# Kernel tuning notes

Hardware: AMD Instinct MI355X
Metric: run time of the kernel (lower is better)

## Reference

```python
import jax, jax.numpy as jnp
import numpy as np

N = 50000          # nodes
E = 3_200_000      # edges (radius-graph topology, avg degree ~64)
C = 10             # node channels
ED = 4             # edge_dim: [dist, dx, dy, food_flag]
H = 16             # message hidden dim
RADIUS = 0.05
ACC_SCALE = 0.005
MAX_VEL = 0.02
EDGES_TO_STAY_ALIVE = 3
CONSUMPTION_EDGES_REQUIRED = 3
NOISE_SCALE = 0.004


def setup_inputs() -> dict:
    key = jax.random.key(0)
    ks = jax.random.split(key, 10)
    pos = jax.random.uniform(ks[0], (N, 2), minval=-1.0, maxval=1.0)
    vel = jax.random.uniform(ks[1], (N, 2), minval=-MAX_VEL, maxval=MAX_VEL)
    # column 4: 1.0 = living cell, 0.0 = food node
    is_cell = (jax.random.uniform(ks[2], (N,)) > 0.2).astype(jnp.float32)
    hidden = jax.random.normal(ks[3], (N, C - 5)) * 0.1
    x = jnp.concatenate([pos, vel, is_cell[:, None], hidden], axis=1)  # [N,10]
    src = jax.random.randint(ks[4], (E,), 0, N)
    dst = jax.random.randint(ks[5], (E,), 0, N)
    noise = jax.random.uniform(ks[6], (N, 2))  # uniform [0,1), mapped to [-1,1) inside
    W_edge = jax.random.normal(ks[7], (ED, H)) * 0.3
    W_src = jax.random.normal(ks[8], (C, H)) * 0.3
    b1 = jnp.zeros((H,), jnp.float32)
    W_out = jax.random.normal(ks[9], (H, 4)) * 0.3
    b2 = jnp.zeros((4,), jnp.float32)
    return dict(x=x, src=src, dst=dst, noise=noise, W_edge=W_edge,
                W_src=W_src, b1=b1, W_out=W_out, b2=b2)


def reference(x, src, dst, noise, W_edge, W_src, b1, W_out, b2):
    pos = x[:, :2]
    vel = x[:, 2:4]
    cell = x[:, 4]
    c_mask = (cell == 1.0).astype(x.dtype)          # [N]

    # ---- edge attributes of the (dynamic) radius graph ----
    d = pos[src] - pos[dst]                          # [E,2] gather
    dist = jnp.sqrt(jnp.sum(d * d, axis=1) + 1e-12)  # [E]
    food_flag = cell[src]                            # 0 for food-source edges
    edge_attr = jnp.concatenate([dist[:, None], d, food_flag[:, None]], axis=1)  # [E,4]

    # ---- message passing: per-edge MLP + scatter-sum + node readout ----
    m = jax.nn.relu(edge_attr @ W_edge + x[src] @ W_src + b1)     # [E,H]
    agg = jax.ops.segment_sum(m, dst, num_segments=N)             # [N,H]
    h = jnp.tanh(agg @ W_out + b2) * c_mask[:, None]              # [N,4], masked as in update_graph

    # ---- velocity / position update ----
    acc = h[:, :2] * ACC_SCALE
    new_vel = jnp.clip(vel + acc, -MAX_VEL, MAX_VEL)
    new_pos = pos + new_vel                                       # wrap_around = False
    vel_noisy = new_vel + (noise * 2.0 - 1.0) * NOISE_SCALE * c_mask[:, None]
    new_x = jnp.concatenate(
        [new_pos, vel_noisy, cell[:, None], h[:, 2:], x[:, 7:]], axis=1)  # [N,10]

    # ---- costs / stats ----
    eps = 1e-6
    border_mask = (jnp.abs(new_pos) > 1.0).astype(x.dtype)        # [N,2]
    border_cost = jnp.sum(jnp.log(jnp.abs(new_pos) + eps) * border_mask)
    food_edge = (food_flag == 0.0)
    visible_food = food_edge.sum()
    mean_food_dist = jnp.sum(dist * food_edge.astype(x.dtype))

    # ---- node removal masks (jit-safe: return keep mask instead of slicing) ----
    deg = jax.ops.segment_sum(jnp.ones_like(dist), dst, num_segments=N)
    dead = (cell == 1.0) & (deg < EDGES_TO_STAY_ALIVE)
    consume_e = (dist < RADIUS) & (cell[src] == 1.0) & (cell[dst] == 0.0)
    cdeg = jax.ops.segment_sum(consume_e.astype(x.dtype), dst, num_segments=N)
    consumed = (cell == 0.0) & (cdeg >= CONSUMPTION_EDGES_REQUIRED)
    keep_mask = ~(dead | consumed)

    velocity_bonus = jnp.mean(jnp.abs(new_vel), axis=0)           # [2]
    dead_cost = dead.sum()
    food_reward = consumed.sum()
    return (new_x, keep_mask, velocity_bonus, border_cost, food_reward,
            dead_cost, visible_food, mean_food_dist)
```

## Files before the change

kernel.cpp:

```cpp
#include <hip/hip_runtime.h>
#include <hip/hip_fp16.h>
#include <math.h>

#define NN 50000
#define NE 3200000

#define NT    128
#define TSZ   392
#define CAP   26624
#define SCB   625
#define EPB   5120
#define EPT   20
#define NSL   6

static constexpr float ACC_SCALE   = 0.005f;
static constexpr float MAX_VEL     = 0.02f;
static constexpr float NOISE_SCALE = 0.004f;
static constexpr float RADIUS      = 0.05f;

#define OUT_KEEP   500000
#define OUT_SCAL   550000

#define WS_SREC  0
#define WS_GCUR  802816
#define WS_BK    804864
#define WS_PACC  4212736
#define WS_PDEG  5416960

__global__ __launch_bounds__(256) void k1_prep(
    const float* __restrict__ x,
    const float* __restrict__ W_edge,
    const float* __restrict__ W_src,
    const float* __restrict__ b1,
    float4* __restrict__ srec,
    int* __restrict__ gcur,
    float* __restrict__ out_scalars)
{
    int n = blockIdx.x * 256 + threadIdx.x;
    if (blockIdx.x == 0) {
        if (threadIdx.x < 7) out_scalars[threadIdx.x] = 0.0f;
        for (int i = threadIdx.x; i < NT * 16; i += 256)
            gcur[i] = (i & 15) ? 0 : (i >> 4) * CAP;
    }
    if (n >= NN) return;

    float xr[10];
#pragma unroll
    for (int c = 0; c < 10; ++c) xr[c] = x[n * 10 + c];
    float cell = xr[4];

    float v[16];
#pragma unroll
    for (int j = 0; j < 16; ++j) {
        float a = fmaf(cell, W_edge[48 + j], b1[j]);
#pragma unroll
        for (int c = 0; c < 10; ++c) a = fmaf(xr[c], W_src[c * 16 + j], a);
        v[j] = a;
    }

    float4 r1, r2;
    r1.x = __builtin_bit_cast(float, __floats2half2_rn(v[0],  v[1]));
    r1.y = __builtin_bit_cast(float, __floats2half2_rn(v[2],  v[3]));
    r1.z = __builtin_bit_cast(float, __floats2half2_rn(v[4],  v[5]));
    r1.w = __builtin_bit_cast(float, __floats2half2_rn(v[6],  v[7]));
    r2.x = __builtin_bit_cast(float, __floats2half2_rn(v[8],  v[9]));
    r2.y = __builtin_bit_cast(float, __floats2half2_rn(v[10], v[11]));
    r2.z = __builtin_bit_cast(float, __floats2half2_rn(v[12], v[13]));
    r2.w = __builtin_bit_cast(float, __floats2half2_rn(v[14], v[15]));

    srec[(size_t)n * 4 + 0] = make_float4(xr[0], xr[1], cell, 0.0f);
    srec[(size_t)n * 4 + 1] = r1;
    srec[(size_t)n * 4 + 2] = r2;
}

__global__ __launch_bounds__(256) void k_scatter(
    const int* __restrict__ src,
    const int* __restrict__ dst,
    int* __restrict__ gcur,
    unsigned* __restrict__ bucket)
{
    __shared__ unsigned stage[EPB];
    __shared__ int hist[NT], binstart[NT], lcur[NT], gbase[NT];
    __shared__ int scanbuf[128];

    int tid = threadIdx.x;
    for (int i = tid; i < NT; i += 256) { hist[i] = 0; lcur[i] = 0; }
    __syncthreads();

    int e0 = blockIdx.x * EPB;

    int d[EPT];
#pragma unroll
    for (int j = 0; j < EPT; ++j) d[j] = dst[e0 + j * 256 + tid];
#pragma unroll
    for (int j = 0; j < EPT; ++j) atomicAdd(&hist[d[j] / TSZ], 1);
    __syncthreads();

    if (tid < 128) scanbuf[tid] = hist[tid];
    __syncthreads();
    for (int off = 1; off < 128; off <<= 1) {
        int v = 0;
        if (tid < 128 && tid >= off) v = scanbuf[tid - off];
        __syncthreads();
        if (tid < 128) scanbuf[tid] += v;
        __syncthreads();
    }
    if (tid < 128) {
        int tt = (tid + blockIdx.x) & 127;
        int bs = scanbuf[tt] - hist[tt];
        binstart[tt] = bs;
        gbase[tt] = atomicAdd(&gcur[tt * 16], hist[tt]) - bs;
    }
    __syncthreads();

    int sreg[EPT];
#pragma unroll
    for (int j = 0; j < EPT; ++j) sreg[j] = src[e0 + j * 256 + tid];
#pragma unroll
    for (int j = 0; j < EPT; ++j) {
        int t  = d[j] / TSZ;
        int dl = d[j] - t * TSZ;
        int pos = binstart[t] + atomicAdd(&lcur[t], 1);
        stage[pos] = (unsigned)sreg[j] | ((unsigned)dl << 16)
                   | ((unsigned)t << 25);
    }
    __syncthreads();

#pragma unroll
    for (int j = 0; j < EPT; ++j) {
        int i = j * 256 + tid;
        unsigned e = stage[i];
        int b = e >> 25;
        int g = gbase[b] + i;
        if (g < (b + 1) * CAP) __builtin_nontemporal_store(e, &bucket[g]);
    }
}

__global__ __launch_bounds__(256, 2) void k_agg(
    const float* __restrict__ W_edge,
    const float* __restrict__ W_out,
    const float4* __restrict__ srec,
    const int* __restrict__ gcur,
    const unsigned* __restrict__ bucket,
    float4* __restrict__ pacc,
    int* __restrict__ pdeg,
    float* __restrict__ out_scalars)
{
    __shared__ float  sAcc[TSZ][5];
    __shared__ int    sDeg[TSZ];
    __shared__ float4 sNI[TSZ];
    __shared__ float  sRed[4][2];

    int t   = blockIdx.x / NSL;
    int sl  = blockIdx.x - t * NSL;
    int tid = threadIdx.x;

    for (int j = tid; j < TSZ; j += 256) {
        int g = t * TSZ + j;
        sNI[j] = (g < NN) ? srec[(size_t)g * 4]
                          : make_float4(9e9f, 9e9f, -1.f, 0.f);
        sAcc[j][0] = 0.f; sAcc[j][1] = 0.f; sAcc[j][2] = 0.f; sAcc[j][3] = 0.f;
        sDeg[j] = 0;
    }

    float w0[16], w1[16], w2[16], woa[16], wob[16], woc[16], wod[16];
#pragma unroll
    for (int k = 0; k < 16; ++k) {
        w0[k] = W_edge[k];
        w1[k] = W_edge[16 + k];
        w2[k] = W_edge[32 + k];
        woa[k] = W_out[k * 4 + 0];
        wob[k] = W_out[k * 4 + 1];
        woc[k] = W_out[k * 4 + 2];
        wod[k] = W_out[k * 4 + 3];
    }
    __syncthreads();

    int cnt = gcur[t * 16] - t * CAP;
    if (cnt > CAP) cnt = CAP;
    int per = (cnt + NSL - 1) / NSL;
    int i0 = sl * per;
    int i1 = min(i0 + per, cnt);

    const unsigned* bk = bucket + (size_t)t * CAP;
    float vis = 0.f, fd = 0.f;

    auto PROC = [&](unsigned e, float4 A, float4 B, float4 C) {
        int dl = (e >> 16) & 0x1FF;
        float4 ni = sNI[dl];
        float dx = A.x - ni.x;
        float dy = A.y - ni.y;
        float dist = sqrtf(fmaf(dx, dx, fmaf(dy, dy, 1e-12f)));

        bool food0 = (A.z == 0.0f);
        vis += food0 ? 1.f : 0.f;
        fd  += food0 ? dist : 0.f;

        bool consume = (dist < RADIUS) && (A.z == 1.0f) && (ni.z == 0.0f);
        atomicAdd(&sDeg[dl], consume ? 65537 : 1);

        float sv[16];
        float2 f;
        f = __half22float2(__builtin_bit_cast(__half2, B.x)); sv[0]=f.x;  sv[1]=f.y;
        f = __half22float2(__builtin_bit_cast(__half2, B.y)); sv[2]=f.x;  sv[3]=f.y;
        f = __half22float2(__builtin_bit_cast(__half2, B.z)); sv[4]=f.x;  sv[5]=f.y;
        f = __half22float2(__builtin_bit_cast(__half2, B.w)); sv[6]=f.x;  sv[7]=f.y;
        f = __half22float2(__builtin_bit_cast(__half2, C.x)); sv[8]=f.x;  sv[9]=f.y;
        f = __half22float2(__builtin_bit_cast(__half2, C.y)); sv[10]=f.x; sv[11]=f.y;
        f = __half22float2(__builtin_bit_cast(__half2, C.z)); sv[12]=f.x; sv[13]=f.y;
        f = __half22float2(__builtin_bit_cast(__half2, C.w)); sv[14]=f.x; sv[15]=f.y;

        float v0 = 0.f, v1 = 0.f, v2 = 0.f, v3 = 0.f;
#pragma unroll
        for (int k = 0; k < 16; ++k) {
            float m = fmaf(dist, w0[k], fmaf(dx, w1[k], fmaf(dy, w2[k], sv[k])));
            m = fmaxf(m, 0.0f);
            v0 = fmaf(m, woa[k], v0);
            v1 = fmaf(m, wob[k], v1);
            v2 = fmaf(m, woc[k], v2);
            v3 = fmaf(m, wod[k], v3);
        }
        atomicAdd(&sAcc[dl][0], v0);
        atomicAdd(&sAcc[dl][1], v1);
        atomicAdd(&sAcc[dl][2], v2);
        atomicAdd(&sAcc[dl][3], v3);
    };

#pragma unroll 1
    for (int base = i0 + tid; base < i1; base += 1024) {
        int iend = i1 - 1;
        int j1 = min(base + 256, iend);
        int j2 = min(base + 512, iend);
        int j3 = min(base + 768, iend);

        unsigned e0 = __builtin_nontemporal_load(&bk[base]);
        unsigned e1 = __builtin_nontemporal_load(&bk[j1]);
        unsigned e2 = __builtin_nontemporal_load(&bk[j2]);
        unsigned e3 = __builtin_nontemporal_load(&bk[j3]);

        const float4* p0 = srec + (size_t)(e0 & 0xFFFF) * 4;
        const float4* p1 = srec + (size_t)(e1 & 0xFFFF) * 4;
        const float4* p2 = srec + (size_t)(e2 & 0xFFFF) * 4;
        const float4* p3 = srec + (size_t)(e3 & 0xFFFF) * 4;
        float4 A0 = p0[0], B0 = p0[1], C0 = p0[2];
        float4 A1 = p1[0], B1 = p1[1], C1 = p1[2];
        float4 A2 = p2[0], B2 = p2[1], C2 = p2[2];
        float4 A3 = p3[0], B3 = p3[1], C3 = p3[2];

        PROC(e0, A0, B0, C0);
        if (base + 256 < i1) PROC(e1, A1, B1, C1);
        if (base + 512 < i1) PROC(e2, A2, B2, C2);
        if (base + 768 < i1) PROC(e3, A3, B3, C3);
    }
    __syncthreads();

    for (int j = tid; j < TSZ; j += 256) {
        int o = sl * (NT * TSZ) + t * TSZ + j;
        pacc[o] = make_float4(sAcc[j][0], sAcc[j][1], sAcc[j][2], sAcc[j][3]);
        pdeg[o] = sDeg[j];
    }

#pragma unroll
    for (int off = 32; off > 0; off >>= 1) {
        vis += __shfl_down(vis, off);
        fd  += __shfl_down(fd,  off);
    }
    int lane = tid & 63, wv = tid >> 6;
    if (lane == 0) { sRed[wv][0] = vis; sRed[wv][1] = fd; }
    __syncthreads();
    if (tid == 0) {
        float a = 0.f, b = 0.f;
#pragma unroll
        for (int wq = 0; wq < 4; ++wq) { a += sRed[wq][0]; b += sRed[wq][1]; }
        atomicAdd(&out_scalars[5], a);
        atomicAdd(&out_scalars[6], b);
    }
}

__global__ __launch_bounds__(256) void k_final(
    const float* __restrict__ x,
    const float* __restrict__ noise,
    const float* __restrict__ b2,
    const float4* __restrict__ pacc,
    const int* __restrict__ pdeg,
    float* __restrict__ out,
    float* __restrict__ out_scalars)
{
    __shared__ float sRed[4][5];
    int tid  = threadIdx.x;
    int n    = blockIdx.x * 128 + (tid >> 1);
    int half = tid & 1;

    float a0 = 0.f, a1 = 0.f, a2 = 0.f, a3 = 0.f;
    int dp = 0;
    if (n < NN) {
#pragma unroll
        for (int k = 0; k < NSL / 2; ++k) {
            int o = (2 * k + half) * (NT * TSZ) + n;
            float4 q = pacc[o];
            a0 += q.x; a1 += q.y; a2 += q.z; a3 += q.w;
            dp += pdeg[o];
        }
    }
    a0 += __shfl_xor(a0, 1);
    a1 += __shfl_xor(a1, 1);
    a2 += __shfl_xor(a2, 1);
    a3 += __shfl_xor(a3, 1);
    dp += __shfl_xor(dp, 1);

    float avx = 0.f, avy = 0.f, bc = 0.f, deadf = 0.f, consf = 0.f;
    if (n < NN && half == 0) {
        float cell = x[n * 10 + 4];
        float cm = (cell == 1.0f) ? 1.0f : 0.0f;
        float h0 = tanhf(a0 + b2[0]) * cm;
        float h1 = tanhf(a1 + b2[1]) * cm;
        float h2 = tanhf(a2 + b2[2]) * cm;
        float h3 = tanhf(a3 + b2[3]) * cm;

        float px = x[n * 10 + 0], py = x[n * 10 + 1];
        float vx = x[n * 10 + 2], vy = x[n * 10 + 3];

        float nvx = fminf(fmaxf(fmaf(h0, ACC_SCALE, vx), -MAX_VEL), MAX_VEL);
        float nvy = fminf(fmaxf(fmaf(h1, ACC_SCALE, vy), -MAX_VEL), MAX_VEL);
        float npx = px + nvx;
        float npy = py + nvy;

        float vnx = nvx + (noise[n * 2 + 0] * 2.0f - 1.0f) * NOISE_SCALE * cm;
        float vny = nvy + (noise[n * 2 + 1] * 2.0f - 1.0f) * NOISE_SCALE * cm;

        float* row = out + (size_t)n * 10;
        row[0] = npx;  row[1] = npy;
        row[2] = vnx;  row[3] = vny;
        row[4] = cell; row[5] = h2;  row[6] = h3;
        row[7] = x[n * 10 + 7];
        row[8] = x[n * 10 + 8];
        row[9] = x[n * 10 + 9];

        float apx = fabsf(npx), apy = fabsf(npy);
        if (apx > 1.0f) bc += logf(apx + 1e-6f);
        if (apy > 1.0f) bc += logf(apy + 1e-6f);

        int deg  = dp & 0xFFFF;
        int cdeg = dp >> 16;
        bool dead = (cell == 1.0f) && (deg < 3);
        bool cons = (cell == 0.0f) && (cdeg >= 3);
        out[OUT_KEEP + n] = (dead || cons) ? 0.0f : 1.0f;
        deadf = dead ? 1.0f : 0.0f;
        consf = cons ? 1.0f : 0.0f;
        avx = fabsf(nvx) * (1.0f / NN);
        avy = fabsf(nvy) * (1.0f / NN);
    }

    float r[5] = { avx, avy, bc, consf, deadf };
#pragma unroll
    for (int q = 0; q < 5; ++q) {
#pragma unroll
        for (int off = 32; off > 0; off >>= 1)
            r[q] += __shfl_down(r[q], off);
    }
    int lane = tid & 63, wv = tid >> 6;
    if (lane == 0) {
#pragma unroll
        for (int q = 0; q < 5; ++q) sRed[wv][q] = r[q];
    }
    __syncthreads();
    if (tid == 0) {
#pragma unroll
        for (int q = 0; q < 5; ++q) {
            float acc = sRed[0][q] + sRed[1][q] + sRed[2][q] + sRed[3][q];
            atomicAdd(&out_scalars[q], acc);
        }
    }
}

extern "C" void kernel_launch(void* const* d_in, const int* in_sizes, int n_in,
                              void* d_out, int out_size, void* d_ws, size_t ws_size,
                              hipStream_t stream) {
    const float* x      = (const float*)d_in[0];
    const int*   src    = (const int*)  d_in[1];
    const int*   dst    = (const int*)  d_in[2];
    const float* noise  = (const float*)d_in[3];
    const float* W_edge = (const float*)d_in[4];
    const float* W_src  = (const float*)d_in[5];
    const float* b1     = (const float*)d_in[6];
    const float* W_out  = (const float*)d_in[7];
    const float* b2     = (const float*)d_in[8];

    float* ws = (float*)d_ws;
    float4*   srec   = (float4*)(ws + WS_SREC);
    int*      gcur   = (int*)(ws + WS_GCUR);
    unsigned* bucket = (unsigned*)(ws + WS_BK);
    float4*   pacc   = (float4*)(ws + WS_PACC);
    int*      pdeg   = (int*)(ws + WS_PDEG);

    float* out         = (float*)d_out;
    float* out_scalars = out + OUT_SCAL;

    k1_prep<<<196, 256, 0, stream>>>(
        x, W_edge, W_src, b1, srec, gcur, out_scalars);

    k_scatter<<<SCB, 256, 0, stream>>>(src, dst, gcur, bucket);

    k_agg<<<NT * NSL, 256, 0, stream>>>(
        W_edge, W_out, srec, gcur, bucket, pacc, pdeg, out_scalars);

    k_final<<<392, 256, 0, stream>>>(
        x, noise, b2, pacc, pdeg, out, out_scalars);
}
```

Baseline: 216.7 us.

## Use 512 smaller dst tiles and fuse node finalization into aggregation kernel

Destination nodes are split into 512 tiles of 98 instead of 128 tiles of 392 processed by 6 slices each. Each tile is now handled entirely by one block, so the partial accumulators and the separate k_final kernel are dropped and the node update plus reductions run at the end of k_agg. The scatter prefix scan is rewritten as a wave-shuffle scan over 512 bins. This removes one launch and the partial-sum round trip through global memory. In exchange each aggregation block has less work, there are more scatter bins, and each bucket's capacity is tighter.

```diff
diff --git a/kernel.cpp b/kernel.cpp
--- a/kernel.cpp
+++ b/kernel.cpp
@@ -5,13 +5,12 @@
 #define NN 50000
 #define NE 3200000
 
-#define NT    128
-#define TSZ   392
-#define CAP   26624
+#define NT    512
+#define TSZ   98
+#define CAP   7168
 #define SCB   625
 #define EPB   5120
 #define EPT   20
-#define NSL   6
 
 static constexpr float ACC_SCALE   = 0.005f;
 static constexpr float MAX_VEL     = 0.02f;
@@ -23,9 +22,7 @@
 
 #define WS_SREC  0
 #define WS_GCUR  802816
-#define WS_BK    804864
-#define WS_PACC  4212736
-#define WS_PDEG  5416960
+#define WS_BK    811008
 
 __global__ __launch_bounds__(256) void k1_prep(
     const float* __restrict__ x,
@@ -81,7 +78,6 @@
 {
     __shared__ unsigned stage[EPB];
     __shared__ int hist[NT], binstart[NT], lcur[NT], gbase[NT];
-    __shared__ int scanbuf[128];
 
     int tid = threadIdx.x;
     for (int i = tid; i < NT; i += 256) { hist[i] = 0; lcur[i] = 0; }
@@ -96,20 +92,25 @@
     for (int j = 0; j < EPT; ++j) atomicAdd(&hist[d[j] / TSZ], 1);
     __syncthreads();
 
-    if (tid < 128) scanbuf[tid] = hist[tid];
-    __syncthreads();
-    for (int off = 1; off < 128; off <<= 1) {
-        int v = 0;
-        if (tid < 128 && tid >= off) v = scanbuf[tid - off];
-        __syncthreads();
-        if (tid < 128) scanbuf[tid] += v;
-        __syncthreads();
-    }
-    if (tid < 128) {
-        int tt = (tid + blockIdx.x) & 127;
-        int bs = scanbuf[tt] - hist[tt];
-        binstart[tt] = bs;
-        gbase[tt] = atomicAdd(&gcur[tt * 16], hist[tt]) - bs;
+    if (tid < 64) {
+        int ps[8]; int s = 0;
+#pragma unroll
+        for (int q = 0; q < 8; ++q) { ps[q] = s; s += hist[tid * 8 + q]; }
+        int incl = s;
+#pragma unroll
+        for (int off = 1; off < 64; off <<= 1) {
+            int v = __shfl_up(incl, off);
+            if (tid >= off) incl += v;
+        }
+        int excl = incl - s;
+#pragma unroll
+        for (int q = 0; q < 8; ++q) binstart[tid * 8 + q] = excl + ps[q];
+    }
+    __syncthreads();
+
+    for (int i = tid; i < NT; i += 256) {
+        int tt = (i + blockIdx.x) & (NT - 1);
+        gbase[tt] = atomicAdd(&gcur[tt * 16], hist[tt]) - binstart[tt];
     }
     __syncthreads();
 
@@ -122,7 +123,7 @@
         int dl = d[j] - t * TSZ;
         int pos = binstart[t] + atomicAdd(&lcur[t], 1);
         stage[pos] = (unsigned)sreg[j] | ((unsigned)dl << 16)
-                   | ((unsigned)t << 25);
+                   | ((unsigned)t << 23);
     }
     __syncthreads();
 
@@ -130,7 +131,7 @@
     for (int j = 0; j < EPT; ++j) {
         int i = j * 256 + tid;
         unsigned e = stage[i];
-        int b = e >> 25;
+        int b = e >> 23;
         int g = gbase[b] + i;
         if (g < (b + 1) * CAP) __builtin_nontemporal_store(e, &bucket[g]);
     }
@@ -139,28 +140,30 @@
 __global__ __launch_bounds__(256, 2) void k_agg(
     const float* __restrict__ W_edge,
     const float* __restrict__ W_out,
+    const float* __restrict__ x,
+    const float* __restrict__ noise,
+    const float* __restrict__ b2,
     const float4* __restrict__ srec,
     const int* __restrict__ gcur,
     const unsigned* __restrict__ bucket,
-    float4* __restrict__ pacc,
-    int* __restrict__ pdeg,
+    float* __restrict__ out,
     float* __restrict__ out_scalars)
 {
     __shared__ float  sAcc[TSZ][5];
     __shared__ int    sDeg[TSZ];
     __shared__ float4 sNI[TSZ];
-    __shared__ float  sRed[4][2];
-
-    int t   = blockIdx.x / NSL;
-    int sl  = blockIdx.x - t * NSL;
+    __shared__ float  sRed[4][7];
+
+    int t   = blockIdx.x;
     int tid = threadIdx.x;
 
-    for (int j = tid; j < TSZ; j += 256) {
-        int g = t * TSZ + j;
-        sNI[j] = (g < NN) ? srec[(size_t)g * 4]
-                          : make_float4(9e9f, 9e9f, -1.f, 0.f);
-        sAcc[j][0] = 0.f; sAcc[j][1] = 0.f; sAcc[j][2] = 0.f; sAcc[j][3] = 0.f;
-        sDeg[j] = 0;
+    if (tid < TSZ) {
+        int g = t * TSZ + tid;
+        sNI[tid] = (g < NN) ? srec[(size_t)g * 4]
+                            : make_float4(9e9f, 9e9f, -1.f, 0.f);
+        sAcc[tid][0] = 0.f; sAcc[tid][1] = 0.f;
+        sAcc[tid][2] = 0.f; sAcc[tid][3] = 0.f;
+        sDeg[tid] = 0;
     }
 
     float w0[16], w1[16], w2[16], woa[16], wob[16], woc[16], wod[16];
@@ -178,15 +181,12 @@
 
     int cnt = gcur[t * 16] - t * CAP;
     if (cnt > CAP) cnt = CAP;
-    int per = (cnt + NSL - 1) / NSL;
-    int i0 = sl * per;
-    int i1 = min(i0 + per, cnt);
 
     const unsigned* bk = bucket + (size_t)t * CAP;
     float vis = 0.f, fd = 0.f;
 
     auto PROC = [&](unsigned e, float4 A, float4 B, float4 C) {
-        int dl = (e >> 16) & 0x1FF;
+        int dl = (e >> 16) & 0x7F;
         float4 ni = sNI[dl];
         float dx = A.x - ni.x;
         float dy = A.y - ni.y;
@@ -227,8 +227,8 @@
     };
 
 #pragma unroll 1
-    for (int base = i0 + tid; base < i1; base += 1024) {
-        int iend = i1 - 1;
+    for (int base = tid; base < cnt; base += 1024) {
+        int iend = cnt - 1;
         int j1 = min(base + 256, iend);
         int j2 = min(base + 512, iend);
         int j3 = min(base + 768, iend);
@@ -248,74 +248,21 @@
         float4 A3 = p3[0], B3 = p3[1], C3 = p3[2];
 
         PROC(e0, A0, B0, C0);
-        if (base + 256 < i1) PROC(e1, A1, B1, C1);
-        if (base + 512 < i1) PROC(e2, A2, B2, C2);
-        if (base + 768 < i1) PROC(e3, A3, B3, C3);
-    }
-    __syncthreads();
-
-    for (int j = tid; j < TSZ; j += 256) {
-        int o = sl * (NT * TSZ) + t * TSZ + j;
-        pacc[o] = make_float4(sAcc[j][0], sAcc[j][1], sAcc[j][2], sAcc[j][3]);
-        pdeg[o] = sDeg[j];
-    }
-
-#pragma unroll
-    for (int off = 32; off > 0; off >>= 1) {
-        vis += __shfl_down(vis, off);
-        fd  += __shfl_down(fd,  off);
-    }
-    int lane = tid & 63, wv = tid >> 6;
-    if (lane == 0) { sRed[wv][0] = vis; sRed[wv][1] = fd; }
-    __syncthreads();
-    if (tid == 0) {
-        float a = 0.f, b = 0.f;
-#pragma unroll
-        for (int wq = 0; wq < 4; ++wq) { a += sRed[wq][0]; b += sRed[wq][1]; }
-        atomicAdd(&out_scalars[5], a);
-        atomicAdd(&out_scalars[6], b);
-    }
-}
-
-__global__ __launch_bounds__(256) void k_final(
-    const float* __restrict__ x,
-    const float* __restrict__ noise,
-    const float* __restrict__ b2,
-    const float4* __restrict__ pacc,
-    const int* __restrict__ pdeg,
-    float* __restrict__ out,
-    float* __restrict__ out_scalars)
-{
-    __shared__ float sRed[4][5];
-    int tid  = threadIdx.x;
-    int n    = blockIdx.x * 128 + (tid >> 1);
-    int half = tid & 1;
-
-    float a0 = 0.f, a1 = 0.f, a2 = 0.f, a3 = 0.f;
-    int dp = 0;
-    if (n < NN) {
-#pragma unroll
-        for (int k = 0; k < NSL / 2; ++k) {
-            int o = (2 * k + half) * (NT * TSZ) + n;
-            float4 q = pacc[o];
-            a0 += q.x; a1 += q.y; a2 += q.z; a3 += q.w;
-            dp += pdeg[o];
-        }
-    }
-    a0 += __shfl_xor(a0, 1);
-    a1 += __shfl_xor(a1, 1);
-    a2 += __shfl_xor(a2, 1);
-    a3 += __shfl_xor(a3, 1);
-    dp += __shfl_xor(dp, 1);
+        if (base + 256 < cnt) PROC(e1, A1, B1, C1);
+        if (base + 512 < cnt) PROC(e2, A2, B2, C2);
+        if (base + 768 < cnt) PROC(e3, A3, B3, C3);
+    }
+    __syncthreads();
 
     float avx = 0.f, avy = 0.f, bc = 0.f, deadf = 0.f, consf = 0.f;
-    if (n < NN && half == 0) {
+    int n = t * TSZ + tid;
+    if (tid < TSZ && n < NN) {
         float cell = x[n * 10 + 4];
         float cm = (cell == 1.0f) ? 1.0f : 0.0f;
-        float h0 = tanhf(a0 + b2[0]) * cm;
-        float h1 = tanhf(a1 + b2[1]) * cm;
-        float h2 = tanhf(a2 + b2[2]) * cm;
-        float h3 = tanhf(a3 + b2[3]) * cm;
+        float h0 = tanhf(sAcc[tid][0] + b2[0]) * cm;
+        float h1 = tanhf(sAcc[tid][1] + b2[1]) * cm;
+        float h2 = tanhf(sAcc[tid][2] + b2[2]) * cm;
+        float h3 = tanhf(sAcc[tid][3] + b2[3]) * cm;
 
         float px = x[n * 10 + 0], py = x[n * 10 + 1];
         float vx = x[n * 10 + 2], vy = x[n * 10 + 3];
@@ -340,6 +287,7 @@
         if (apx > 1.0f) bc += logf(apx + 1e-6f);
         if (apy > 1.0f) bc += logf(apy + 1e-6f);
 
+        int dp = sDeg[tid];
         int deg  = dp & 0xFFFF;
         int cdeg = dp >> 16;
         bool dead = (cell == 1.0f) && (deg < 3);
@@ -351,9 +299,9 @@
         avy = fabsf(nvy) * (1.0f / NN);
     }
 
-    float r[5] = { avx, avy, bc, consf, deadf };
-#pragma unroll
-    for (int q = 0; q < 5; ++q) {
+    float r[7] = { avx, avy, bc, consf, deadf, vis, fd };
+#pragma unroll
+    for (int q = 0; q < 7; ++q) {
 #pragma unroll
         for (int off = 32; off > 0; off >>= 1)
             r[q] += __shfl_down(r[q], off);
@@ -361,12 +309,12 @@
     int lane = tid & 63, wv = tid >> 6;
     if (lane == 0) {
 #pragma unroll
-        for (int q = 0; q < 5; ++q) sRed[wv][q] = r[q];
+        for (int q = 0; q < 7; ++q) sRed[wv][q] = r[q];
     }
     __syncthreads();
     if (tid == 0) {
 #pragma unroll
-        for (int q = 0; q < 5; ++q) {
+        for (int q = 0; q < 7; ++q) {
             float acc = sRed[0][q] + sRed[1][q] + sRed[2][q] + sRed[3][q];
             atomicAdd(&out_scalars[q], acc);
         }
@@ -390,8 +338,6 @@
     float4*   srec   = (float4*)(ws + WS_SREC);
     int*      gcur   = (int*)(ws + WS_GCUR);
     unsigned* bucket = (unsigned*)(ws + WS_BK);
-    float4*   pacc   = (float4*)(ws + WS_PACC);
-    int*      pdeg   = (int*)(ws + WS_PDEG);
 
     float* out         = (float*)d_out;
     float* out_scalars = out + OUT_SCAL;
@@ -401,9 +347,6 @@
 
     k_scatter<<<SCB, 256, 0, stream>>>(src, dst, gcur, bucket);
 
-    k_agg<<<NT * NSL, 256, 0, stream>>>(
-        W_edge, W_out, srec, gcur, bucket, pacc, pdeg, out_scalars);
-
-    k_final<<<392, 256, 0, stream>>>(
-        x, noise, b2, pacc, pdeg, out, out_scalars);
+    k_agg<<<NT, 256, 0, stream>>>(
+        W_edge, W_out, x, noise, b2, srec, gcur, bucket, out, out_scalars);
 }
```

After: 231.1 us. +6.6%, slower.
